# Kernel optimization log

Measured on AMD Instinct MI355X. Metric: run time of the kernel, lower is better.

Reference implementation:

```python
import jax, jax.numpy as jnp
import numpy as np

N_NODES = 100000
N_EDGES = 3200000
NUM_FEATURES = 1433
HIDDEN = 16
NUM_CLASSES = 7


def setup_inputs() -> dict:
    key = jax.random.key(0)
    k1, k2, k3, k4, k5, k6 = jax.random.split(key, 6)
    x = jax.random.normal(k1, (N_NODES, NUM_FEATURES), dtype=jnp.float32)
    edge_index = jax.random.randint(k2, (2, N_EDGES), 0, N_NODES, dtype=jnp.int64)
    # Glorot-ish init for the two GCN layer weights + zero biases
    W1 = jax.random.normal(k3, (NUM_FEATURES, HIDDEN), dtype=jnp.float32) / np.sqrt(NUM_FEATURES)
    b1 = jnp.zeros((HIDDEN,), dtype=jnp.float32)
    W2 = jax.random.normal(k4, (HIDDEN, NUM_CLASSES), dtype=jnp.float32) / np.sqrt(HIDDEN)
    b2 = jnp.zeros((NUM_CLASSES,), dtype=jnp.float32)
    return {"x": x, "edge_index": edge_index, "W1": W1, "b1": b1, "W2": W2, "b2": b2}


def _gcn_conv(x, W, b, src, dst, deg_inv_sqrt, n_nodes):
    # PyG GCNConv: h = D^{-1/2}(A+I)D^{-1/2} (x W) + b
    h = x @ W                                   # [N, out]
    coef = deg_inv_sqrt[src] * deg_inv_sqrt[dst]  # [E]
    msg = h[src] * coef[:, None]                # gather + scale, [E, out]
    agg = jax.ops.segment_sum(msg, dst, num_segments=n_nodes)  # scatter-add
    return agg + b


def reference(x, edge_index, W1, b1, W2, b2):
    n = x.shape[0]
    loops = jnp.arange(n, dtype=edge_index.dtype)
    src = jnp.concatenate([edge_index[0], loops])  # add self-loops
    dst = jnp.concatenate([edge_index[1], loops])
    deg = jax.ops.segment_sum(jnp.ones_like(dst, dtype=x.dtype), dst, num_segments=n)
    deg_inv_sqrt = jnp.where(deg > 0, jax.lax.rsqrt(deg), 0.0)

    h = _gcn_conv(x, W1, b1, src, dst, deg_inv_sqrt, n)
    h = jax.nn.relu(h)
    h = _gcn_conv(h, W2, b2, src, dst, deg_inv_sqrt, n)
    h = jax.nn.relu(h)
    return jax.nn.log_softmax(h, axis=1)
```

## Files before the change

kernel.cpp:

```cpp
#include <hip/hip_runtime.h>
#include <hip/hip_bf16.h>
#include <math.h>

#define NF 1433
#define NH 16
#define NC 7
#define NCH 45
#define NBKT_MAX 512
#define SC_C 3072
#define CAP 9216

typedef __attribute__((ext_vector_type(8))) short bf16x8;
typedef __attribute__((ext_vector_type(4))) float f32x4;

__device__ __forceinline__ unsigned short f2bf(float f) {
  unsigned int u = __float_as_uint(f);
  unsigned int r = (u + 0x7FFFu + ((u >> 16) & 1u)) >> 16;
  return (unsigned short)r;
}
__device__ __forceinline__ short f2bfs(float f) {
  union { __hip_bfloat16 h; short s; } u;
  u.h = __float2bfloat16(f);
  return u.s;
}
__device__ __forceinline__ unsigned int packbf(float lo, float hi) {
  return (unsigned int)f2bf(lo) | ((unsigned int)f2bf(hi) << 16);
}
__device__ __forceinline__ void acc8(float* a, uint4 r) {
  a[0] += __uint_as_float(r.x << 16); a[1] += __uint_as_float(r.x & 0xffff0000u);
  a[2] += __uint_as_float(r.y << 16); a[3] += __uint_as_float(r.y & 0xffff0000u);
  a[4] += __uint_as_float(r.z << 16); a[5] += __uint_as_float(r.z & 0xffff0000u);
  a[6] += __uint_as_float(r.w << 16); a[7] += __uint_as_float(r.w & 0xffff0000u);
}
__device__ __forceinline__ void acc8f(float* a, uint4 r, float c) {
  a[0] = fmaf(__uint_as_float(r.x << 16), c, a[0]);
  a[1] = fmaf(__uint_as_float(r.x & 0xffff0000u), c, a[1]);
  a[2] = fmaf(__uint_as_float(r.y << 16), c, a[2]);
  a[3] = fmaf(__uint_as_float(r.y & 0xffff0000u), c, a[3]);
  a[4] = fmaf(__uint_as_float(r.z << 16), c, a[4]);
  a[5] = fmaf(__uint_as_float(r.z & 0xffff0000u), c, a[5]);
  a[6] = fmaf(__uint_as_float(r.w << 16), c, a[6]);
  a[7] = fmaf(__uint_as_float(r.w & 0xffff0000u), c, a[7]);
}

#define GLOAD(gp, lp) __builtin_amdgcn_global_load_lds(                     \
    (const __attribute__((address_space(1))) void*)(gp),                    \
    (__attribute__((address_space(3))) void*)(lp), 4, 0, 0)

#define SEP() asm volatile("" ::: "memory")

__global__ void k_prep(const float* __restrict__ W1, short* __restrict__ Wb,
                       int* __restrict__ bfill) {
  int t = blockIdx.x * blockDim.x + threadIdx.x;
  if (t < NBKT_MAX) bfill[t * 16] = t * CAP;
  if (t >= NCH * 64 * 8) return;
  int i = t & 7, l = (t >> 3) & 63, c = t >> 9;
  int g = l >> 4, col = l & 15;
  int k = c * 32 + g * 8 + i;
  float v = (k < NF) ? W1[(size_t)k * NH + col] : 0.f;
  Wb[t] = (short)f2bf(v);
}

__global__ __launch_bounds__(256) void k_fused(
    const float* __restrict__ x, const short* __restrict__ Wb,
    const int* __restrict__ ei, int* __restrict__ bfill,
    int* __restrict__ ebuf, unsigned short* __restrict__ hs1,
    int n, int E, int nbkt, int nsb) {
  __shared__ __align__(16) char smem[49664];
  int blk = blockIdx.x, t = threadIdx.x;

  if (blk < nsb) {
    int* h   = (int*)smem;
    int* lo  = h + NBKT_MAX;
    int* lb  = lo + NBKT_MAX;
    int* sc2 = lb + NBKT_MAX;
    int* sval = sc2 + 256;
    unsigned short* sbkt = (unsigned short*)(sval + SC_C);
    const int* src = ei;
    const int* dst = ei + E;
    for (int i = t; i < NBKT_MAX; i += 256) h[i] = 0;
    __syncthreads();
    int e0 = blk * SC_C;
    int e1 = min(E, e0 + SC_C);
    int csize = e1 - e0;
    for (int e = e0 + t; e < e1; e += 256)
      atomicAdd(&h[((unsigned)dst[e]) >> 8], 1);
    __syncthreads();
    int base = 0;
#pragma unroll
    for (int j = 0; j < 2; ++j) {
      int idx = j * 256 + t;
      int v = h[idx];
      sc2[t] = v;
      __syncthreads();
      for (int o = 1; o < 256; o <<= 1) {
        int u = (t >= o) ? sc2[t - o] : 0;
        __syncthreads();
        sc2[t] += u;
        __syncthreads();
      }
      lo[idx] = base + sc2[t] - v;
      int tot = sc2[255];
      __syncthreads();
      base += tot;
    }
    for (int i = t; i < nbkt; i += 256) {
      int c = h[i];
      lb[i] = c ? atomicAdd(&bfill[i * 16], c) : 0;
      h[i] = 0;
    }
    __syncthreads();
    for (int e = e0 + t; e < e1; e += 256) {
      unsigned d = (unsigned)dst[e];
      int bk = d >> 8;
      int p = lo[bk] + atomicAdd(&h[bk], 1);
      sval[p] = (int)(((d & 255u) << 24) | (unsigned)src[e]);
      sbkt[p] = (unsigned short)bk;
    }
    __syncthreads();
    for (int i = t; i < csize; i += 256) {
      int bk = sbkt[i];
      ebuf[lb[bk] + (i - lo[bk])] = sval[i];
    }
    return;
  }

  float* xsf = (float*)smem;
#define XIDX(B, ROW, COL) ((((B) * 16 + (ROW)) * 388) + (COL))
  int l = t & 63, wv = t >> 6;
  int row0 = (blk - nsb) << 4;
  int rl = l & 15, g = l >> 4;

  const bf16x8* wp = (const bf16x8*)Wb + l;
  f32x4 acc;
#pragma unroll
  for (int j = 0; j < 4; ++j) acc[j] = 0.f;

  const float* rp[4];
#pragma unroll
  for (int r = 0; r < 4; ++r) {
    int row = row0 + 4 * wv + r;
    rp[r] = x + (size_t)((row < n) ? row : (n - 1)) * NF;
  }

#define STAGE6(M0, B) do {                                                   \
    _Pragma("unroll") for (int r = 0; r < 4; ++r)                            \
    _Pragma("unroll") for (int j = 0; j < 6; ++j)                            \
      GLOAD(rp[r] + (M0) + j * 64 + l, xsf + XIDX(B, 4 * wv + r, j * 64));   \
  } while (0)

#define DOCHUNK(B, CC, WREG) do {                                            \
    const float4* p = (const float4*)(xsf + XIDX(B, rl, (CC) * 32 + g * 8)); \
    float4 a0 = p[0], a1 = p[1];                                             \
    bf16x8 af;                                                               \
    af[0] = f2bfs(a0.x); af[1] = f2bfs(a0.y);                                \
    af[2] = f2bfs(a0.z); af[3] = f2bfs(a0.w);                                \
    af[4] = f2bfs(a1.x); af[5] = f2bfs(a1.y);                                \
    af[6] = f2bfs(a1.z); af[7] = f2bfs(a1.w);                                \
    acc = __builtin_amdgcn_mfma_f32_16x16x32_bf16(af, WREG, acc, 0, 0, 0);   \
  } while (0)

  STAGE6(0, 0);
  bf16x8 w0 = wp[(size_t)(wv) * 64];
  bf16x8 w1 = wp[(size_t)(wv + 4) * 64];
  bf16x8 w2 = wp[(size_t)(wv + 8) * 64];
  STAGE6(384, 1);
  asm volatile("s_waitcnt vmcnt(24) lgkmcnt(0)" ::: "memory");
  __builtin_amdgcn_s_barrier();
  DOCHUNK(0, wv, w0); DOCHUNK(0, wv + 4, w1); DOCHUNK(0, wv + 8, w2);
  __builtin_amdgcn_s_barrier();
  w0 = wp[(size_t)(12 + wv) * 64];
  w1 = wp[(size_t)(16 + wv) * 64];
  w2 = wp[(size_t)(20 + wv) * 64];
  STAGE6(768, 0);
  asm volatile("s_waitcnt vmcnt(24) lgkmcnt(0)" ::: "memory");
  __builtin_amdgcn_s_barrier();
  DOCHUNK(1, wv, w0); DOCHUNK(1, wv + 4, w1); DOCHUNK(1, wv + 8, w2);
  __builtin_amdgcn_s_barrier();
  w0 = wp[(size_t)(24 + wv) * 64];
  w1 = wp[(size_t)(28 + wv) * 64];
  w2 = wp[(size_t)(32 + wv) * 64];
#pragma unroll
  for (int r = 0; r < 4; ++r) {
#pragma unroll
    for (int j = 0; j < 4; ++j)
      GLOAD(rp[r] + 1152 + j * 64 + l, xsf + XIDX(1, 4 * wv + r, j * 64));
    GLOAD(rp[r] + (NF - 64) + l, xsf + XIDX(1, 4 * wv + r, 217));
  }
  if (l < 28) xsf[XIDX(1, 4 * wv + (l / 7), 281 + (l % 7))] = 0.f;
  asm volatile("s_waitcnt vmcnt(20) lgkmcnt(0)" ::: "memory");
  __builtin_amdgcn_s_barrier();
  DOCHUNK(0, wv, w0); DOCHUNK(0, wv + 4, w1); DOCHUNK(0, wv + 8, w2);
  __builtin_amdgcn_s_barrier();
  w0 = wp[(size_t)(36 + wv) * 64];
  w1 = wp[(size_t)(40 + wv) * 64];
  bf16x8 w2b = wp[(size_t)44 * 64];
  asm volatile("s_waitcnt vmcnt(0) lgkmcnt(0)" ::: "memory");
  __builtin_amdgcn_s_barrier();
  DOCHUNK(1, wv, w0); DOCHUNK(1, wv + 4, w1);
  if (wv == 0) DOCHUNK(1, 8, w2b);
  __syncthreads();

  float* ps = xsf;
#pragma unroll
  for (int r = 0; r < 4; ++r)
    ps[(wv * 16 + g * 4 + r) * 16 + rl] = acc[r];
  __syncthreads();
  if (wv == 0) {
    int row = l >> 2, c0 = (l & 3) * 4;
    float4 s0 = *(const float4*)&ps[(row) * 16 + c0];
    float4 s1 = *(const float4*)&ps[(16 + row) * 16 + c0];
    float4 s2 = *(const float4*)&ps[(32 + row) * 16 + c0];
    float4 s3 = *(const float4*)&ps[(48 + row) * 16 + c0];
    int grow = row0 + row;
    if (grow < n) {
      ushort4 o;
      o.x = f2bf(s0.x + s1.x + s2.x + s3.x);
      o.y = f2bf(s0.y + s1.y + s2.y + s3.y);
      o.z = f2bf(s0.z + s1.z + s2.z + s3.z);
      o.w = f2bf(s0.w + s1.w + s2.w + s3.w);
      *(ushort4*)(hs1 + (size_t)grow * NH + c0) = o;
    }
  }
#undef STAGE6
#undef DOCHUNK
#undef XIDX
}

__global__ __launch_bounds__(256) void k_bcsr(const int* __restrict__ ebuf,
                                              const int* __restrict__ bfill,
                                              int* __restrict__ off,
                                              int* __restrict__ end,
                                              int* __restrict__ srcs,
                                              float* __restrict__ dis, int n) {
  __shared__ int h[256];
  __shared__ int sc[256];
  int b = blockIdx.x, t = threadIdx.x;
  int eb = b * CAP, ee = bfill[b * 16];
  h[t] = 0;
  __syncthreads();
  for (int i = eb + t; i < ee; i += 256)
    atomicAdd(&h[((unsigned)ebuf[i]) >> 24], 1);
  __syncthreads();
  int deg = h[t];
  sc[t] = deg;
  __syncthreads();
  for (int o = 1; o < 256; o <<= 1) {
    int u = (t >= o) ? sc[t - o] : 0;
    __syncthreads();
    sc[t] += u;
    __syncthreads();
  }
  int excl = sc[t] - deg;
  int node = (b << 8) + t;
  if (node < n) {
    off[node] = eb + excl;
    end[node] = eb + excl + deg;
    dis[node] = rsqrtf((float)deg + 1.0f);
  }
  h[t] = eb + excl;
  __syncthreads();
  for (int i = eb + t; i < ee; i += 256) {
    unsigned v = (unsigned)ebuf[i];
    int slot = atomicAdd(&h[v >> 24], 1);
    srcs[slot] = (int)(v & 0xFFFFFFu);
  }
}

__global__ __launch_bounds__(256) void k_pull1(
    const int* __restrict__ off, const int* __restrict__ end,
    const int* __restrict__ srcs, const float* __restrict__ dis,
    const uint4* __restrict__ hs1, const float* __restrict__ b1,
    const float* __restrict__ W2, uint4* __restrict__ hs2, int n) {
  int t = blockIdx.x * blockDim.x + threadIdx.x;
  int d = t >> 4;
  if (d >= n) return;
  int sub = t & 15, half = sub & 1, ph = sub >> 1;
  float dd = dis[d];

  float a[8] = {0.f, 0.f, 0.f, 0.f, 0.f, 0.f, 0.f, 0.f};
  if (ph == 0) acc8f(a, hs1[(size_t)d * 2 + half], dd);

  int k = off[d] + ph, k1 = end[d];
  for (; k + 8 < k1; k += 16) {
    int s0 = srcs[k], s1 = srcs[k + 8];
    float c0 = dis[s0], c1 = dis[s1];
    uint4 r0 = hs1[(size_t)s0 * 2 + half];
    uint4 r1 = hs1[(size_t)s1 * 2 + half];
    acc8f(a, r0, c0);
    acc8f(a, r1, c1);
  }
  if (k < k1) {
    int s = srcs[k];
    acc8f(a, hs1[(size_t)s * 2 + half], dis[s]);
  }

#pragma unroll
  for (int i = 0; i < 8; ++i) {
    a[i] += __shfl_xor(a[i], 2);
    a[i] += __shfl_xor(a[i], 4);
    a[i] += __shfl_xor(a[i], 8);
  }

  float v[8];
#pragma unroll
  for (int i = 0; i < 8; ++i) v[i] = fmaxf(a[i] * dd + b1[half * 8 + i], 0.f);
  float p[NC];
#pragma unroll
  for (int c = 0; c < NC; ++c) {
    float s = 0.f;
#pragma unroll
    for (int i = 0; i < 8; ++i) s = fmaf(v[i], W2[(half * 8 + i) * NC + c], s);
    p[c] = s;
  }
#pragma unroll
  for (int c = 0; c < NC; ++c) p[c] += __shfl_xor(p[c], 1);
  if (sub == 0) {
    uint4 o;
    o.x = packbf(p[0] * dd, p[1] * dd);
    o.y = packbf(p[2] * dd, p[3] * dd);
    o.z = packbf(p[4] * dd, p[5] * dd);
    o.w = packbf(p[6] * dd, 0.f);
    hs2[d] = o;
  }
}

__global__ __launch_bounds__(256) void k_pull2(
    const int* __restrict__ off, const int* __restrict__ end,
    const int* __restrict__ srcs, const float* __restrict__ dis,
    const uint4* __restrict__ hs2, const float* __restrict__ b2,
    float* __restrict__ out, int n) {
  int t = blockIdx.x * blockDim.x + threadIdx.x;
  int d = t >> 3;
  if (d >= n) return;
  int ph = t & 7;

  float a[8] = {0.f, 0.f, 0.f, 0.f, 0.f, 0.f, 0.f, 0.f};
  if (ph == 0) acc8(a, hs2[d]);

  int k = off[d] + ph, k1 = end[d];
  for (; k + 8 < k1; k += 16) {
    int s0 = srcs[k], s1 = srcs[k + 8];
    uint4 r0 = hs2[s0];
    uint4 r1 = hs2[s1];
    acc8(a, r0);
    acc8(a, r1);
  }
  if (k < k1) acc8(a, hs2[srcs[k]]);

#pragma unroll
  for (int i = 0; i < 8; ++i) {
    a[i] += __shfl_xor(a[i], 1);
    a[i] += __shfl_xor(a[i], 2);
    a[i] += __shfl_xor(a[i], 4);
  }
  float dd = dis[d];
  float u[NC];
#pragma unroll
  for (int c = 0; c < NC; ++c) u[c] = fmaxf(a[c] * dd + b2[c], 0.f);
  float m = u[0];
#pragma unroll
  for (int c = 1; c < NC; ++c) m = fmaxf(m, u[c]);
  float sum = 0.f;
#pragma unroll
  for (int c = 0; c < NC; ++c) sum += expf(u[c] - m);
  float lg = logf(sum);
  if (ph < NC) out[(size_t)d * NC + ph] = u[ph] - m - lg;
}

extern "C" void kernel_launch(void* const* d_in, const int* in_sizes, int n_in,
                              void* d_out, int out_size, void* d_ws, size_t ws_size,
                              hipStream_t stream) {
  const float* x  = (const float*)d_in[0];
  const int*   ei = (const int*)d_in[1];
  const float* W1 = (const float*)d_in[2];
  const float* b1 = (const float*)d_in[3];
  const float* W2 = (const float*)d_in[4];
  const float* b2 = (const float*)d_in[5];
  int n = in_sizes[0] / NF;
  int E = in_sizes[1] / 2;
  int nbkt = (n + 255) >> 8;

  char* w = (char*)d_ws;
#define TAKE(ptrty, name, bytes) \
  ptrty name = (ptrty)w; w += ((size_t)(bytes) + 15) & ~(size_t)15;
  TAKE(unsigned short*, hs1,  sizeof(short) * (size_t)n * NH)
  TAKE(uint4*,          hs2,  16 * (size_t)n)
  TAKE(float*,          dis,  sizeof(float) * n)
  TAKE(short*,          Wb,   sizeof(short) * NCH * 64 * 8)
  TAKE(int*,            bfill,sizeof(int) * 16 * NBKT_MAX)
  TAKE(int*,            ebuf, sizeof(int) * (size_t)NBKT_MAX * CAP)
  TAKE(int*,            off,  sizeof(int) * n)
  TAKE(int*,            end,  sizeof(int) * n)
  TAKE(int*,            srcs, sizeof(int) * (size_t)NBKT_MAX * CAP)
#undef TAKE
  float* out = (float*)d_out;

  int nsb = (E + SC_C - 1) / SC_C;
  int ntb = (n + 15) / 16;

  k_prep<<<(NCH * 64 * 8 + 255) / 256, 256, 0, stream>>>(W1, Wb, bfill);

  k_fused<<<nsb + ntb, 256, 0, stream>>>(x, Wb, ei, bfill, ebuf, hs1,
                                         n, E, nbkt, nsb);

  k_bcsr<<<nbkt, 256, 0, stream>>>(ebuf, bfill, off, end, srcs, dis, n);
  k_pull1<<<((size_t)n * 16 + 255) / 256, 256, 0, stream>>>(
      off, end, srcs, dis, (const uint4*)hs1, b1, W2, hs2, n);
  k_pull2<<<((size_t)n * 8 + 255) / 256, 256, 0, stream>>>(
      off, end, srcs, dis, hs2, b2, out, n);
}
```

Baseline: 269.9 us.

## Fuse CSR bucket build and first pull aggregation via grid-wide barrier

Merges the bucket-to-CSR kernel and the layer-1 pull kernel into one kernel. Each block builds its 256-node CSR segment in shared memory, writes it out, then waits on a global atomic barrier so every node's dis value is visible before aggregating. The block then aggregates from its shared-memory source list, cutting one launch and the global reread of srcs/off/end. The cost is that all nbkt (~391) blocks must be co-resident or the spin barrier deadlocks. The 36KB+ of LDS per block also limits occupancy in the pull phase.

New measurement: 316.4 us. +17.2%, slower.

```diff
diff --git a/kernel.cpp b/kernel.cpp
--- a/kernel.cpp
+++ b/kernel.cpp
@@ -47,12 +47,11 @@
     (const __attribute__((address_space(1))) void*)(gp),                    \
     (__attribute__((address_space(3))) void*)(lp), 4, 0, 0)
 
-#define SEP() asm volatile("" ::: "memory")
-
 __global__ void k_prep(const float* __restrict__ W1, short* __restrict__ Wb,
-                       int* __restrict__ bfill) {
+                       int* __restrict__ bfill, int* __restrict__ bar) {
   int t = blockIdx.x * blockDim.x + threadIdx.x;
   if (t < NBKT_MAX) bfill[t * 16] = t * CAP;
+  if (t < 16) bar[t] = 0;
   if (t >= NCH * 64 * 8) return;
   int i = t & 7, l = (t >> 3) & 63, c = t >> 9;
   int g = l >> 4, col = l & 15;
@@ -227,101 +226,114 @@
 #undef XIDX
 }
 
-__global__ __launch_bounds__(256) void k_bcsr(const int* __restrict__ ebuf,
-                                              const int* __restrict__ bfill,
-                                              int* __restrict__ off,
-                                              int* __restrict__ end,
-                                              int* __restrict__ srcs,
-                                              float* __restrict__ dis, int n) {
-  __shared__ int h[256];
-  __shared__ int sc[256];
+__global__ __launch_bounds__(256) void k_csrpull1(
+    const int* __restrict__ ebuf, const int* __restrict__ bfill,
+    const uint4* __restrict__ hs1, const float* __restrict__ b1,
+    const float* __restrict__ W2, int* __restrict__ off,
+    int* __restrict__ end, int* __restrict__ srcs, float* __restrict__ dis,
+    uint4* __restrict__ hs2, int* __restrict__ bar, int n, int nbkt) {
+  __shared__ int s_src[CAP];
+  __shared__ int s_off[256];
+  __shared__ int s_cur[256];
+  __shared__ int s_deg[256];
   int b = blockIdx.x, t = threadIdx.x;
-  int eb = b * CAP, ee = bfill[b * 16];
-  h[t] = 0;
-  __syncthreads();
-  for (int i = eb + t; i < ee; i += 256)
-    atomicAdd(&h[((unsigned)ebuf[i]) >> 24], 1);
-  __syncthreads();
-  int deg = h[t];
-  sc[t] = deg;
+  int eb = b * CAP;
+  int cnt = bfill[b * 16] - eb;
+
+  s_cur[t] = 0;
+  __syncthreads();
+  for (int i = t; i < cnt; i += 256)
+    atomicAdd(&s_cur[((unsigned)ebuf[eb + i]) >> 24], 1);
+  __syncthreads();
+  int deg = s_cur[t];
+  s_off[t] = deg;
   __syncthreads();
   for (int o = 1; o < 256; o <<= 1) {
-    int u = (t >= o) ? sc[t - o] : 0;
-    __syncthreads();
-    sc[t] += u;
-    __syncthreads();
-  }
-  int excl = sc[t] - deg;
+    int u = (t >= o) ? s_off[t - o] : 0;
+    __syncthreads();
+    s_off[t] += u;
+    __syncthreads();
+  }
+  int excl = s_off[t] - deg;
   int node = (b << 8) + t;
   if (node < n) {
     off[node] = eb + excl;
     end[node] = eb + excl + deg;
     dis[node] = rsqrtf((float)deg + 1.0f);
   }
-  h[t] = eb + excl;
-  __syncthreads();
-  for (int i = eb + t; i < ee; i += 256) {
-    unsigned v = (unsigned)ebuf[i];
-    int slot = atomicAdd(&h[v >> 24], 1);
-    srcs[slot] = (int)(v & 0xFFFFFFu);
-  }
-}
-
-__global__ __launch_bounds__(256) void k_pull1(
-    const int* __restrict__ off, const int* __restrict__ end,
-    const int* __restrict__ srcs, const float* __restrict__ dis,
-    const uint4* __restrict__ hs1, const float* __restrict__ b1,
-    const float* __restrict__ W2, uint4* __restrict__ hs2, int n) {
-  int t = blockIdx.x * blockDim.x + threadIdx.x;
-  int d = t >> 4;
-  if (d >= n) return;
-  int sub = t & 15, half = sub & 1, ph = sub >> 1;
-  float dd = dis[d];
-
-  float a[8] = {0.f, 0.f, 0.f, 0.f, 0.f, 0.f, 0.f, 0.f};
-  if (ph == 0) acc8f(a, hs1[(size_t)d * 2 + half], dd);
-
-  int k = off[d] + ph, k1 = end[d];
-  for (; k + 8 < k1; k += 16) {
-    int s0 = srcs[k], s1 = srcs[k + 8];
-    float c0 = dis[s0], c1 = dis[s1];
-    uint4 r0 = hs1[(size_t)s0 * 2 + half];
-    uint4 r1 = hs1[(size_t)s1 * 2 + half];
-    acc8f(a, r0, c0);
-    acc8f(a, r1, c1);
-  }
-  if (k < k1) {
-    int s = srcs[k];
-    acc8f(a, hs1[(size_t)s * 2 + half], dis[s]);
-  }
-
-#pragma unroll
-  for (int i = 0; i < 8; ++i) {
-    a[i] += __shfl_xor(a[i], 2);
-    a[i] += __shfl_xor(a[i], 4);
-    a[i] += __shfl_xor(a[i], 8);
-  }
-
-  float v[8];
-#pragma unroll
-  for (int i = 0; i < 8; ++i) v[i] = fmaxf(a[i] * dd + b1[half * 8 + i], 0.f);
-  float p[NC];
-#pragma unroll
-  for (int c = 0; c < NC; ++c) {
-    float s = 0.f;
-#pragma unroll
-    for (int i = 0; i < 8; ++i) s = fmaf(v[i], W2[(half * 8 + i) * NC + c], s);
-    p[c] = s;
-  }
-#pragma unroll
-  for (int c = 0; c < NC; ++c) p[c] += __shfl_xor(p[c], 1);
-  if (sub == 0) {
-    uint4 o;
-    o.x = packbf(p[0] * dd, p[1] * dd);
-    o.y = packbf(p[2] * dd, p[3] * dd);
-    o.z = packbf(p[4] * dd, p[5] * dd);
-    o.w = packbf(p[6] * dd, 0.f);
-    hs2[d] = o;
+  __syncthreads();
+  s_off[t] = excl;
+  s_cur[t] = excl;
+  s_deg[t] = deg;
+  __syncthreads();
+  for (int i = t; i < cnt; i += 256) {
+    unsigned v = (unsigned)ebuf[eb + i];
+    int slot = atomicAdd(&s_cur[v >> 24], 1);
+    s_src[slot] = (int)(v & 0xFFFFFFu);
+  }
+  __syncthreads();
+  for (int i = t; i < cnt; i += 256) srcs[eb + i] = s_src[i];
+
+  __syncthreads();
+  if (t == 0) {
+    __threadfence();
+    __hip_atomic_fetch_add(bar, 1, __ATOMIC_RELEASE, __HIP_MEMORY_SCOPE_AGENT);
+    while (__hip_atomic_load(bar, __ATOMIC_ACQUIRE, __HIP_MEMORY_SCOPE_AGENT) < nbkt)
+      __builtin_amdgcn_s_sleep(8);
+  }
+  __syncthreads();
+
+#pragma unroll 1
+  for (int pass = 0; pass < 16; ++pass) {
+    int idx = pass * 16 + (t >> 4);
+    int sub = t & 15, half = sub & 1, ph = sub >> 1;
+    int d = (b << 8) + idx;
+    int k0 = s_off[idx], dg = s_deg[idx];
+    float dd = rsqrtf((float)dg + 1.0f);
+    float a[8] = {0.f, 0.f, 0.f, 0.f, 0.f, 0.f, 0.f, 0.f};
+    if (d < n) {
+      if (ph == 0) acc8f(a, hs1[(size_t)d * 2 + half], dd);
+      int k = ph, k1 = dg;
+      for (; k + 8 < k1; k += 16) {
+        int s0 = s_src[k0 + k], s1 = s_src[k0 + k + 8];
+        float c0 = dis[s0], c1 = dis[s1];
+        uint4 r0 = hs1[(size_t)s0 * 2 + half];
+        uint4 r1 = hs1[(size_t)s1 * 2 + half];
+        acc8f(a, r0, c0);
+        acc8f(a, r1, c1);
+      }
+      if (k < k1) {
+        int s = s_src[k0 + k];
+        acc8f(a, hs1[(size_t)s * 2 + half], dis[s]);
+      }
+    }
+#pragma unroll
+    for (int i = 0; i < 8; ++i) {
+      a[i] += __shfl_xor(a[i], 2);
+      a[i] += __shfl_xor(a[i], 4);
+      a[i] += __shfl_xor(a[i], 8);
+    }
+    float v[8];
+#pragma unroll
+    for (int i = 0; i < 8; ++i) v[i] = fmaxf(a[i] * dd + b1[half * 8 + i], 0.f);
+    float p[NC];
+#pragma unroll
+    for (int c = 0; c < NC; ++c) {
+      float s = 0.f;
+#pragma unroll
+      for (int i = 0; i < 8; ++i) s = fmaf(v[i], W2[(half * 8 + i) * NC + c], s);
+      p[c] = s;
+    }
+#pragma unroll
+    for (int c = 0; c < NC; ++c) p[c] += __shfl_xor(p[c], 1);
+    if (sub == 0 && d < n) {
+      uint4 o;
+      o.x = packbf(p[0] * dd, p[1] * dd);
+      o.y = packbf(p[2] * dd, p[3] * dd);
+      o.z = packbf(p[4] * dd, p[5] * dd);
+      o.w = packbf(p[6] * dd, 0.f);
+      hs2[d] = o;
+    }
   }
 }
 
@@ -389,6 +401,7 @@
   TAKE(float*,          dis,  sizeof(float) * n)
   TAKE(short*,          Wb,   sizeof(short) * NCH * 64 * 8)
   TAKE(int*,            bfill,sizeof(int) * 16 * NBKT_MAX)
+  TAKE(int*,            bar,  sizeof(int) * 16)
   TAKE(int*,            ebuf, sizeof(int) * (size_t)NBKT_MAX * CAP)
   TAKE(int*,            off,  sizeof(int) * n)
   TAKE(int*,            end,  sizeof(int) * n)
@@ -399,14 +412,14 @@
   int nsb = (E + SC_C - 1) / SC_C;
   int ntb = (n + 15) / 16;
 
-  k_prep<<<(NCH * 64 * 8 + 255) / 256, 256, 0, stream>>>(W1, Wb, bfill);
+  k_prep<<<(NCH * 64 * 8 + 255) / 256, 256, 0, stream>>>(W1, Wb, bfill, bar);
 
   k_fused<<<nsb + ntb, 256, 0, stream>>>(x, Wb, ei, bfill, ebuf, hs1,
                                          n, E, nbkt, nsb);
 
-  k_bcsr<<<nbkt, 256, 0, stream>>>(ebuf, bfill, off, end, srcs, dis, n);
-  k_pull1<<<((size_t)n * 16 + 255) / 256, 256, 0, stream>>>(
-      off, end, srcs, dis, (const uint4*)hs1, b1, W2, hs2, n);
+  k_csrpull1<<<nbkt, 256, 0, stream>>>(ebuf, bfill, (const uint4*)hs1, b1, W2,
+                                       off, end, srcs, dis, hs2, bar, n, nbkt);
+
   k_pull2<<<((size_t)n * 8 + 255) / 256, 256, 0, stream>>>(
       off, end, srcs, dis, hs2, b2, out, n);
 }
```

## Halve bucket width and stage CSR bucket sort through LDS

Applied to the files above, without the earlier changes.

Dest buckets shrink from 256 to 128 nodes (1024 buckets, capacity 4608), which frees a bit so 25-bit source ids fit in the packed word. k_bcsr now loads each bucket's edges into shared memory with vectorized int4 reads, counts and scatters in LDS, then writes srcs back with coalesced int4 stores instead of random global scatter. The cost is about 36KB of LDS per block, which lowers occupancy, plus more buckets and a longer scan in the scatter phase. Only 128 of 256 threads map to nodes.

New measurement: 274.5 us. No clear change (+1.7%).

```diff
diff --git a/kernel.cpp b/kernel.cpp
--- a/kernel.cpp
+++ b/kernel.cpp
@@ -6,9 +6,10 @@
 #define NH 16
 #define NC 7
 #define NCH 45
-#define NBKT_MAX 512
+#define NBKT_MAX 1024
 #define SC_C 3072
-#define CAP 9216
+#define CAP 4608
+#define SMASK 0x1FFFFFFu
 
 typedef __attribute__((ext_vector_type(8))) short bf16x8;
 typedef __attribute__((ext_vector_type(4))) float f32x4;
@@ -46,8 +47,6 @@
 #define GLOAD(gp, lp) __builtin_amdgcn_global_load_lds(                     \
     (const __attribute__((address_space(1))) void*)(gp),                    \
     (__attribute__((address_space(3))) void*)(lp), 4, 0, 0)
-
-#define SEP() asm volatile("" ::: "memory")
 
 __global__ void k_prep(const float* __restrict__ W1, short* __restrict__ Wb,
                        int* __restrict__ bfill) {
@@ -84,11 +83,11 @@
     int e1 = min(E, e0 + SC_C);
     int csize = e1 - e0;
     for (int e = e0 + t; e < e1; e += 256)
-      atomicAdd(&h[((unsigned)dst[e]) >> 8], 1);
+      atomicAdd(&h[((unsigned)dst[e]) >> 7], 1);
     __syncthreads();
     int base = 0;
 #pragma unroll
-    for (int j = 0; j < 2; ++j) {
+    for (int j = 0; j < 4; ++j) {
       int idx = j * 256 + t;
       int v = h[idx];
       sc2[t] = v;
@@ -112,9 +111,9 @@
     __syncthreads();
     for (int e = e0 + t; e < e1; e += 256) {
       unsigned d = (unsigned)dst[e];
-      int bk = d >> 8;
+      int bk = d >> 7;
       int p = lo[bk] + atomicAdd(&h[bk], 1);
-      sval[p] = (int)(((d & 255u) << 24) | (unsigned)src[e]);
+      sval[p] = (int)(((d & 127u) << 25) | (unsigned)src[e]);
       sbkt[p] = (unsigned short)bk;
     }
     __syncthreads();
@@ -233,38 +232,51 @@
                                               int* __restrict__ end,
                                               int* __restrict__ srcs,
                                               float* __restrict__ dis, int n) {
-  __shared__ int h[256];
-  __shared__ int sc[256];
+  __shared__ int s_in[CAP];
+  __shared__ int s_out[CAP];
+  __shared__ int s_cnt[256];
+  __shared__ int s_sc[256];
   int b = blockIdx.x, t = threadIdx.x;
-  int eb = b * CAP, ee = bfill[b * 16];
-  h[t] = 0;
-  __syncthreads();
-  for (int i = eb + t; i < ee; i += 256)
-    atomicAdd(&h[((unsigned)ebuf[i]) >> 24], 1);
-  __syncthreads();
-  int deg = h[t];
-  sc[t] = deg;
+  int eb = b * CAP;
+  int cnt = bfill[b * 16] - eb;
+  int cnt4 = cnt >> 2;
+
+  const int4* e4 = (const int4*)(ebuf + eb);
+  for (int i = t; i < cnt4; i += 256) ((int4*)s_in)[i] = e4[i];
+  for (int i = cnt4 * 4 + t; i < cnt; i += 256) s_in[i] = ebuf[eb + i];
+  s_cnt[t] = 0;
+  __syncthreads();
+  for (int i = t; i < cnt; i += 256)
+    atomicAdd(&s_cnt[((unsigned)s_in[i]) >> 25], 1);
+  __syncthreads();
+  int deg = s_cnt[t];
+  s_sc[t] = deg;
   __syncthreads();
   for (int o = 1; o < 256; o <<= 1) {
-    int u = (t >= o) ? sc[t - o] : 0;
-    __syncthreads();
-    sc[t] += u;
-    __syncthreads();
-  }
-  int excl = sc[t] - deg;
-  int node = (b << 8) + t;
-  if (node < n) {
+    int u = (t >= o) ? s_sc[t - o] : 0;
+    __syncthreads();
+    s_sc[t] += u;
+    __syncthreads();
+  }
+  int excl = s_sc[t] - deg;
+  int node = (b << 7) + t;
+  if (t < 128 && node < n) {
     off[node] = eb + excl;
     end[node] = eb + excl + deg;
     dis[node] = rsqrtf((float)deg + 1.0f);
   }
-  h[t] = eb + excl;
-  __syncthreads();
-  for (int i = eb + t; i < ee; i += 256) {
-    unsigned v = (unsigned)ebuf[i];
-    int slot = atomicAdd(&h[v >> 24], 1);
-    srcs[slot] = (int)(v & 0xFFFFFFu);
-  }
+  __syncthreads();
+  s_cnt[t] = excl;
+  __syncthreads();
+  for (int i = t; i < cnt; i += 256) {
+    unsigned v = (unsigned)s_in[i];
+    int slot = atomicAdd(&s_cnt[v >> 25], 1);
+    s_out[slot] = (int)(v & SMASK);
+  }
+  __syncthreads();
+  int4* sr4 = (int4*)(srcs + eb);
+  for (int i = t; i < cnt4; i += 256) sr4[i] = ((int4*)s_out)[i];
+  for (int i = cnt4 * 4 + t; i < cnt; i += 256) srcs[eb + i] = s_out[i];
 }
 
 __global__ __launch_bounds__(256) void k_pull1(
@@ -379,7 +391,7 @@
   const float* b2 = (const float*)d_in[5];
   int n = in_sizes[0] / NF;
   int E = in_sizes[1] / 2;
-  int nbkt = (n + 255) >> 8;
+  int nbkt = (n + 127) >> 7;
 
   char* w = (char*)d_ws;
 #define TAKE(ptrty, name, bytes) \
```
